# Kernel optimization log

Hardware: AMD Instinct MI355X
Metric: run time of the kernel (lower is better)

## Reference

```python
import jax, jax.numpy as jnp
import numpy as np


def _splat_one(inp, fx, fy):
    """Bilinear forward-splat one sample.
    inp: [C1, H, W] values to scatter; fx, fy: [H, W] destination coords.
    Returns [C1, H, W] scatter-add accumulation.
    """
    C1, H, W = inp.shape
    inp_flat = inp.reshape(C1, H * W)  # [C1, HW]
    out = jnp.zeros((C1, H * W), dtype=inp.dtype)
    x0 = jnp.floor(fx).astype(jnp.int32)
    y0 = jnp.floor(fy).astype(jnp.int32)
    for dx in (0, 1):
        for dy in (0, 1):
            xi = x0 + dx
            yi = y0 + dy
            # bilinear weight to this corner
            w = (1.0 - jnp.abs(fx - xi.astype(fx.dtype))) * (1.0 - jnp.abs(fy - yi.astype(fy.dtype)))
            valid = (xi >= 0) & (xi < W) & (yi >= 0) & (yi < H)
            w = jnp.where(valid, w, 0.0).reshape(-1)  # [HW]
            idx = (jnp.clip(yi, 0, H - 1) * W + jnp.clip(xi, 0, W - 1)).reshape(-1)
            out = out.at[:, idx].add(inp_flat * w[None, :])
    return out.reshape(C1, H, W)


def softsplat_soft(img, flow, metric):
    """Softmax splatting (FunctionSoftsplat, mode='soft').
    img [B,C,H,W], flow [B,2,H,W] (ch0=x disp, ch1=y disp), metric [B,1,H,W].
    """
    B, C, H, W = img.shape
    weight = jnp.exp(metric)                      # [B,1,H,W]
    inp = jnp.concatenate([img * weight, weight], axis=1)  # [B,C+1,H,W]
    gx = jnp.arange(W, dtype=img.dtype)[None, None, :]
    gy = jnp.arange(H, dtype=img.dtype)[None, :, None]
    fx = flow[:, 0] + gx                          # [B,H,W]
    fy = flow[:, 1] + gy                          # [B,H,W]
    acc = jax.vmap(_splat_one)(inp, fx, fy)       # [B,C+1,H,W]
    norm = acc[:, C:C + 1]
    norm = jnp.where(norm == 0.0, 1.0, norm)      # avoid div-by-zero (matches original)
    return acc[:, :C] / norm


def setup_inputs() -> dict:
    key = jax.random.key(0)
    k1, k2, k3 = jax.random.split(key, 3)
    B, C, H, W = 8, 3, 1024, 1024
    img = jax.random.uniform(k1, (B, C, H, W), dtype=jnp.float32)
    flow = jax.random.normal(k2, (B, 2, H, W), dtype=jnp.float32) * 4.0
    metric = jax.random.normal(k3, (B, 1, H, W), dtype=jnp.float32)
    return {"img": img, "flow": flow, "metric": metric}


def reference(img, flow, metric):
    return softsplat_soft(img, flow, metric)
```

## Files before the change

kernel.cpp:

```cpp
#include <hip/hip_runtime.h>
#include <hip/hip_fp16.h>

constexpr int B_ = 8;
constexpr int H_ = 1024;
constexpr int W_ = 1024;
constexpr int HW_ = H_ * W_;

constexpr int TW = 64;
constexpr int TH = 64;
constexpr int R  = 16;
constexpr int WX = TW + 2 * R;
constexpr int WY = TH + 2 * R;
constexpr int NPIX = WX * WY;
constexpr int NT = 1024;
constexpr int LSTRIDE = TW + 1;

constexpr int CAP = 65536;

constexpr size_t OFF_VALS  = 64;
constexpr size_t OFF_CELLS = OFF_VALS + (size_t)CAP * 16;
constexpr size_t OFF_VAL   = OFF_CELLS + (size_t)CAP * 4;

__global__ __launch_bounds__(256) void prepass_kernel(
    const float* __restrict__ img,
    const float* __restrict__ flow,
    const float* __restrict__ metric,
    uint2* __restrict__ val,
    int* __restrict__ counter,
    float4* __restrict__ rec_vals,
    int* __restrict__ rec_cells)
{
    const int t = blockIdx.x * 256 + threadIdx.x;
    if (t >= B_ * HW_ / 4) return;
    const int b  = t >> 18;
    const int p4 = (t & (HW_ / 4 - 1)) << 2;
    const int y  = p4 >> 10;
    const int x0p = p4 & (W_ - 1);

    const float4 m4  = *(const float4*)(metric + (size_t)b * HW_ + p4);
    const float4 i0  = *(const float4*)(img + (size_t)(b * 3 + 0) * HW_ + p4);
    const float4 i1  = *(const float4*)(img + (size_t)(b * 3 + 1) * HW_ + p4);
    const float4 i2  = *(const float4*)(img + (size_t)(b * 3 + 2) * HW_ + p4);
    const float4 fx4 = *(const float4*)(flow + (size_t)(b * 2 + 0) * HW_ + p4);
    const float4 fy4 = *(const float4*)(flow + (size_t)(b * 2 + 1) * HW_ + p4);

    uint2 packed[4];
    const float mv[4] = {m4.x, m4.y, m4.z, m4.w};
    const float a0[4] = {i0.x, i0.y, i0.z, i0.w};
    const float a1[4] = {i1.x, i1.y, i1.z, i1.w};
    const float a2[4] = {i2.x, i2.y, i2.z, i2.w};
    const float fxa[4] = {fx4.x, fx4.y, fx4.z, fx4.w};
    const float fya[4] = {fy4.x, fy4.y, fy4.z, fy4.w};

#pragma unroll
    for (int k = 0; k < 4; ++k) {
        const float wgt = __expf(mv[k]);
        const float v0 = a0[k] * wgt;
        const float v1 = a1[k] * wgt;
        const float v2 = a2[k] * wgt;
        const __half2 h01 = __floats2half2_rn(v0, v1);
        const __half2 h23 = __floats2half2_rn(v2, wgt);
        packed[k].x = *(const unsigned int*)&h01;
        packed[k].y = *(const unsigned int*)&h23;

        const int x = x0p + k;
        const float fx = fxa[k] + (float)x;
        const float fy = fya[k] + (float)y;
        const float x0f = floorf(fx);
        const float y0f = floorf(fy);
        const int x0 = (int)x0f;
        const int y0 = (int)y0f;
        const bool far = (abs(x0 - x) > R) || (abs(x0 + 1 - x) > R) ||
                         (abs(y0 - y) > R) || (abs(y0 + 1 - y) > R);
        if (far) {
            const float wx1 = fx - x0f, wx0 = 1.0f - wx1;
            const float wy1 = fy - y0f, wy0 = 1.0f - wy1;
#pragma unroll
            for (int dy = 0; dy < 2; ++dy) {
                const int yi = y0 + dy;
                if (yi < 0 || yi >= H_) continue;
#pragma unroll
                for (int dx = 0; dx < 2; ++dx) {
                    const int xi = x0 + dx;
                    if (xi < 0 || xi >= W_) continue;
                    if (abs(xi - x) <= R && abs(yi - y) <= R) continue;
                    const float w = (dx ? wx1 : wx0) * (dy ? wy1 : wy0);
                    const int idx = atomicAdd(counter, 1);
                    if (idx < CAP) {
                        rec_cells[idx] = (b << 20) | (yi << 10) | xi;
                        rec_vals[idx]  = make_float4(v0 * w, v1 * w, v2 * w, wgt * w);
                    }
                }
            }
        }
    }
    *(reinterpret_cast<uint4*>(val + (size_t)b * HW_ + p4))     = *(uint4*)&packed[0];
    *(reinterpret_cast<uint4*>(val + (size_t)b * HW_ + p4) + 1) = *(uint4*)&packed[2];
}

__global__ __launch_bounds__(NT) void splat_tile_kernel(
    const float* __restrict__ flow,
    const uint2* __restrict__ val,
    float* __restrict__ out,
    const int* __restrict__ counter,
    const float4* __restrict__ rec_vals,
    const int* __restrict__ rec_cells)
{
    __shared__ float acc[4][TH][LSTRIDE];

    const int tid = threadIdx.x;
    const int tx0 = blockIdx.x * TW;
    const int ty0 = blockIdx.y * TH;
    const int b   = blockIdx.z;

    {
        float4* const a4 = (float4*)&acc[0][0][0];
        const float4 z = make_float4(0.f, 0.f, 0.f, 0.f);
        for (int i = tid; i < 4 * TH * LSTRIDE / 4; i += NT) a4[i] = z;
    }
    __syncthreads();

    const float* const flowx = flow + (size_t)(b * 2 + 0) * HW_;
    const float* const flowy = flow + (size_t)(b * 2 + 1) * HW_;
    const uint2* const valb  = val + (size_t)b * HW_;

    for (int i = tid; i < NPIX; i += NT) {
        const int row = i / WX;
        const int col = i - row * WX;
        const int sy = ty0 - R + row;
        const int sx = tx0 - R + col;
        if ((unsigned)sy >= H_ || (unsigned)sx >= W_) continue;
        const int p = (sy << 10) + sx;

        const float fx = flowx[p] + (float)sx;
        const float fy = flowy[p] + (float)sy;
        const float x0f = floorf(fx);
        const float y0f = floorf(fy);
        const int x0 = (int)x0f;
        const int y0 = (int)y0f;
        if (x0 + 1 < tx0 || x0 > tx0 + TW - 1 ||
            y0 + 1 < ty0 || y0 > ty0 + TH - 1) continue;

        const uint2 u = valb[p];
        const float2 f01 = __half22float2(*(const __half2*)&u.x);
        const float2 f23 = __half22float2(*(const __half2*)&u.y);
        const float v0 = f01.x, v1 = f01.y, v2 = f23.x, wgt = f23.y;

        const float wx1 = fx - x0f, wx0 = 1.0f - wx1;
        const float wy1 = fy - y0f, wy0 = 1.0f - wy1;

#pragma unroll
        for (int dy = 0; dy < 2; ++dy) {
            const int yi = y0 + dy;
            const int ly = yi - ty0;
            if ((unsigned)ly >= TH) continue;
#pragma unroll
            for (int dx = 0; dx < 2; ++dx) {
                const int xi = x0 + dx;
                const int lx = xi - tx0;
                if ((unsigned)lx >= TW) continue;
                if (abs(xi - sx) > R || abs(yi - sy) > R) continue;
                const float w = (dx ? wx1 : wx0) * (dy ? wy1 : wy0);
                unsafeAtomicAdd(&acc[0][ly][lx], v0 * w);
                unsafeAtomicAdd(&acc[1][ly][lx], v1 * w);
                unsafeAtomicAdd(&acc[2][ly][lx], v2 * w);
                unsafeAtomicAdd(&acc[3][ly][lx], wgt * w);
            }
        }
    }
    __syncthreads();

    const int n = min(*counter, CAP);
    for (int r = tid; r < n; r += NT) {
        const int cell = rec_cells[r];
        if ((cell >> 20) != b) continue;
        const int q  = cell & (HW_ - 1);
        const int ly = (q >> 10) - ty0;
        const int lx = (q & (W_ - 1)) - tx0;
        if ((unsigned)ly >= TH || (unsigned)lx >= TW) continue;
        const float4 v = rec_vals[r];
        unsafeAtomicAdd(&acc[0][ly][lx], v.x);
        unsafeAtomicAdd(&acc[1][ly][lx], v.y);
        unsafeAtomicAdd(&acc[2][ly][lx], v.z);
        unsafeAtomicAdd(&acc[3][ly][lx], v.w);
    }
    __syncthreads();

    for (int i = tid; i < TH * TW / 4; i += NT) {
        const int ly  = i >> 4;
        const int lx  = (i & 15) << 2;
        float invs[4];
#pragma unroll
        for (int k = 0; k < 4; ++k) {
            const float wsum = acc[3][ly][lx + k];
            invs[k] = (wsum == 0.0f) ? 1.0f : 1.0f / wsum;
        }
        const float4 o0 = make_float4(acc[0][ly][lx] * invs[0], acc[0][ly][lx+1] * invs[1],
                                      acc[0][ly][lx+2] * invs[2], acc[0][ly][lx+3] * invs[3]);
        const float4 o1 = make_float4(acc[1][ly][lx] * invs[0], acc[1][ly][lx+1] * invs[1],
                                      acc[1][ly][lx+2] * invs[2], acc[1][ly][lx+3] * invs[3]);
        const float4 o2 = make_float4(acc[2][ly][lx] * invs[0], acc[2][ly][lx+1] * invs[1],
                                      acc[2][ly][lx+2] * invs[2], acc[2][ly][lx+3] * invs[3]);
        const int q = ((ty0 + ly) << 10) + tx0 + lx;
        *(float4*)(out + (size_t)(b * 3 + 0) * HW_ + q) = o0;
        *(float4*)(out + (size_t)(b * 3 + 1) * HW_ + q) = o1;
        *(float4*)(out + (size_t)(b * 3 + 2) * HW_ + q) = o2;
    }
}

extern "C" void kernel_launch(void* const* d_in, const int* in_sizes, int n_in,
                              void* d_out, int out_size, void* d_ws, size_t ws_size,
                              hipStream_t stream)
{
    const float* img    = (const float*)d_in[0];
    const float* flow   = (const float*)d_in[1];
    const float* metric = (const float*)d_in[2];
    float* out = (float*)d_out;

    int*    counter   = (int*)d_ws;
    float4* rec_vals  = (float4*)((char*)d_ws + OFF_VALS);
    int*    rec_cells = (int*)((char*)d_ws + OFF_CELLS);
    uint2*  val       = (uint2*)((char*)d_ws + OFF_VAL);

    hipMemsetAsync(counter, 0, 64, stream);

    {
        const int n = B_ * HW_ / 4;
        prepass_kernel<<<(n + 255) / 256, 256, 0, stream>>>(
            img, flow, metric, val, counter, rec_vals, rec_cells);
    }
    {
        dim3 grid(W_ / TW, H_ / TH, B_);
        splat_tile_kernel<<<grid, NT, 0, stream>>>(
            flow, val, out, counter, rec_vals, rec_cells);
    }
}
```

Measured before the change: 731.3 us.

## Drop packed fp16 intermediate; read img and metric directly in splat kernel

The prepass no longer computes and writes a packed half-precision value buffer for every pixel. It now only reads flow and loads img and metric for pixels whose targets fall outside the halo. The tile kernel reads the fp32 img channels and metric directly and recomputes exp per halo pixel. This removes a full write and re-read of an intermediate buffer and the fp16 rounding, at the cost of four separate fp32 gathers and redundant exp work on the overlapping halo region.

```diff
diff --git a/kernel.cpp b/kernel.cpp
--- a/kernel.cpp
+++ b/kernel.cpp
@@ -1,5 +1,4 @@
 #include <hip/hip_runtime.h>
-#include <hip/hip_fp16.h>
 
 constexpr int B_ = 8;
 constexpr int H_ = 1024;
@@ -19,13 +18,11 @@
 
 constexpr size_t OFF_VALS  = 64;
 constexpr size_t OFF_CELLS = OFF_VALS + (size_t)CAP * 16;
-constexpr size_t OFF_VAL   = OFF_CELLS + (size_t)CAP * 4;
-
-__global__ __launch_bounds__(256) void prepass_kernel(
+
+__global__ __launch_bounds__(256) void outlier_kernel(
     const float* __restrict__ img,
     const float* __restrict__ flow,
     const float* __restrict__ metric,
-    uint2* __restrict__ val,
     int* __restrict__ counter,
     float4* __restrict__ rec_vals,
     int* __restrict__ rec_cells)
@@ -37,32 +34,13 @@
     const int y  = p4 >> 10;
     const int x0p = p4 & (W_ - 1);
 
-    const float4 m4  = *(const float4*)(metric + (size_t)b * HW_ + p4);
-    const float4 i0  = *(const float4*)(img + (size_t)(b * 3 + 0) * HW_ + p4);
-    const float4 i1  = *(const float4*)(img + (size_t)(b * 3 + 1) * HW_ + p4);
-    const float4 i2  = *(const float4*)(img + (size_t)(b * 3 + 2) * HW_ + p4);
     const float4 fx4 = *(const float4*)(flow + (size_t)(b * 2 + 0) * HW_ + p4);
     const float4 fy4 = *(const float4*)(flow + (size_t)(b * 2 + 1) * HW_ + p4);
-
-    uint2 packed[4];
-    const float mv[4] = {m4.x, m4.y, m4.z, m4.w};
-    const float a0[4] = {i0.x, i0.y, i0.z, i0.w};
-    const float a1[4] = {i1.x, i1.y, i1.z, i1.w};
-    const float a2[4] = {i2.x, i2.y, i2.z, i2.w};
     const float fxa[4] = {fx4.x, fx4.y, fx4.z, fx4.w};
     const float fya[4] = {fy4.x, fy4.y, fy4.z, fy4.w};
 
 #pragma unroll
     for (int k = 0; k < 4; ++k) {
-        const float wgt = __expf(mv[k]);
-        const float v0 = a0[k] * wgt;
-        const float v1 = a1[k] * wgt;
-        const float v2 = a2[k] * wgt;
-        const __half2 h01 = __floats2half2_rn(v0, v1);
-        const __half2 h23 = __floats2half2_rn(v2, wgt);
-        packed[k].x = *(const unsigned int*)&h01;
-        packed[k].y = *(const unsigned int*)&h23;
-
         const int x = x0p + k;
         const float fx = fxa[k] + (float)x;
         const float fy = fya[k] + (float)y;
@@ -72,35 +50,39 @@
         const int y0 = (int)y0f;
         const bool far = (abs(x0 - x) > R) || (abs(x0 + 1 - x) > R) ||
                          (abs(y0 - y) > R) || (abs(y0 + 1 - y) > R);
-        if (far) {
-            const float wx1 = fx - x0f, wx0 = 1.0f - wx1;
-            const float wy1 = fy - y0f, wy0 = 1.0f - wy1;
-#pragma unroll
-            for (int dy = 0; dy < 2; ++dy) {
-                const int yi = y0 + dy;
-                if (yi < 0 || yi >= H_) continue;
-#pragma unroll
-                for (int dx = 0; dx < 2; ++dx) {
-                    const int xi = x0 + dx;
-                    if (xi < 0 || xi >= W_) continue;
-                    if (abs(xi - x) <= R && abs(yi - y) <= R) continue;
-                    const float w = (dx ? wx1 : wx0) * (dy ? wy1 : wy0);
-                    const int idx = atomicAdd(counter, 1);
-                    if (idx < CAP) {
-                        rec_cells[idx] = (b << 20) | (yi << 10) | xi;
-                        rec_vals[idx]  = make_float4(v0 * w, v1 * w, v2 * w, wgt * w);
-                    }
+        if (!far) continue;
+
+        const int p = p4 + k;
+        const float wgt = __expf(metric[(size_t)b * HW_ + p]);
+        const float v0 = img[(size_t)(b * 3 + 0) * HW_ + p] * wgt;
+        const float v1 = img[(size_t)(b * 3 + 1) * HW_ + p] * wgt;
+        const float v2 = img[(size_t)(b * 3 + 2) * HW_ + p] * wgt;
+        const float wx1 = fx - x0f, wx0 = 1.0f - wx1;
+        const float wy1 = fy - y0f, wy0 = 1.0f - wy1;
+#pragma unroll
+        for (int dy = 0; dy < 2; ++dy) {
+            const int yi = y0 + dy;
+            if (yi < 0 || yi >= H_) continue;
+#pragma unroll
+            for (int dx = 0; dx < 2; ++dx) {
+                const int xi = x0 + dx;
+                if (xi < 0 || xi >= W_) continue;
+                if (abs(xi - x) <= R && abs(yi - y) <= R) continue;
+                const float w = (dx ? wx1 : wx0) * (dy ? wy1 : wy0);
+                const int idx = atomicAdd(counter, 1);
+                if (idx < CAP) {
+                    rec_cells[idx] = (b << 20) | (yi << 10) | xi;
+                    rec_vals[idx]  = make_float4(v0 * w, v1 * w, v2 * w, wgt * w);
                 }
             }
         }
     }
-    *(reinterpret_cast<uint4*>(val + (size_t)b * HW_ + p4))     = *(uint4*)&packed[0];
-    *(reinterpret_cast<uint4*>(val + (size_t)b * HW_ + p4) + 1) = *(uint4*)&packed[2];
 }
 
 __global__ __launch_bounds__(NT) void splat_tile_kernel(
+    const float* __restrict__ img,
     const float* __restrict__ flow,
-    const uint2* __restrict__ val,
+    const float* __restrict__ metric,
     float* __restrict__ out,
     const int* __restrict__ counter,
     const float4* __restrict__ rec_vals,
@@ -122,7 +104,10 @@
 
     const float* const flowx = flow + (size_t)(b * 2 + 0) * HW_;
     const float* const flowy = flow + (size_t)(b * 2 + 1) * HW_;
-    const uint2* const valb  = val + (size_t)b * HW_;
+    const float* const metr  = metric + (size_t)b * HW_;
+    const float* const img0  = img + (size_t)(b * 3 + 0) * HW_;
+    const float* const img1  = img + (size_t)(b * 3 + 1) * HW_;
+    const float* const img2  = img + (size_t)(b * 3 + 2) * HW_;
 
     for (int i = tid; i < NPIX; i += NT) {
         const int row = i / WX;
@@ -141,10 +126,10 @@
         if (x0 + 1 < tx0 || x0 > tx0 + TW - 1 ||
             y0 + 1 < ty0 || y0 > ty0 + TH - 1) continue;
 
-        const uint2 u = valb[p];
-        const float2 f01 = __half22float2(*(const __half2*)&u.x);
-        const float2 f23 = __half22float2(*(const __half2*)&u.y);
-        const float v0 = f01.x, v1 = f01.y, v2 = f23.x, wgt = f23.y;
+        const float wgt = __expf(metr[p]);
+        const float v0 = img0[p] * wgt;
+        const float v1 = img1[p] * wgt;
+        const float v2 = img2[p] * wgt;
 
         const float wx1 = fx - x0f, wx0 = 1.0f - wx1;
         const float wy1 = fy - y0f, wy0 = 1.0f - wy1;
@@ -186,9 +171,9 @@
     }
     __syncthreads();
 
-    for (int i = tid; i < TH * TW / 4; i += NT) {
-        const int ly  = i >> 4;
-        const int lx  = (i & 15) << 2;
+    for (int i2 = tid; i2 < TH * TW / 4; i2 += NT) {
+        const int ly  = i2 >> 4;
+        const int lx  = (i2 & 15) << 2;
         float invs[4];
 #pragma unroll
         for (int k = 0; k < 4; ++k) {
@@ -220,18 +205,17 @@
     int*    counter   = (int*)d_ws;
     float4* rec_vals  = (float4*)((char*)d_ws + OFF_VALS);
     int*    rec_cells = (int*)((char*)d_ws + OFF_CELLS);
-    uint2*  val       = (uint2*)((char*)d_ws + OFF_VAL);
 
     hipMemsetAsync(counter, 0, 64, stream);
 
     {
         const int n = B_ * HW_ / 4;
-        prepass_kernel<<<(n + 255) / 256, 256, 0, stream>>>(
-            img, flow, metric, val, counter, rec_vals, rec_cells);
+        outlier_kernel<<<(n + 255) / 256, 256, 0, stream>>>(
+            img, flow, metric, counter, rec_vals, rec_cells);
     }
     {
         dim3 grid(W_ / TW, H_ / TH, B_);
         splat_tile_kernel<<<grid, NT, 0, stream>>>(
-            flow, val, out, counter, rec_vals, rec_cells);
+            img, flow, metric, out, counter, rec_vals, rec_cells);
     }
 }
```

Result: no change. 725.1 us (-0.9%).
